# Performance work log

Measured on AMD Instinct MI355X. Metric: run time of the kernel, lower is better.

## Reference

```python
import jax, jax.numpy as jnp
import numpy as np

N_NODES = 1_000_000
N_FEATS = 64
KERNEL_SIZE = 3


def setup_inputs() -> dict:
    key = jax.random.key(0)
    kx, kw = jax.random.split(key)
    x = jax.random.normal(kx, (N_NODES, N_FEATS), dtype=jnp.float32)
    # xavier_uniform for weight of shape (kernel_size, n_feats)
    bound = float(np.sqrt(6.0 / (KERNEL_SIZE + N_FEATS)))
    weight = jax.random.uniform(kw, (KERNEL_SIZE, N_FEATS), dtype=jnp.float32,
                                minval=-bound, maxval=bound)
    # sequential -1/+1 neighbor edges (like mlcg.neighbor_list.get_seq_neigh)
    idx = jnp.arange(N_NODES, dtype=jnp.int64) if jax.config.jax_enable_x64 else jnp.arange(N_NODES, dtype=jnp.int32)
    src = jnp.concatenate([idx[:-1], idx[1:]])   # j
    dst = jnp.concatenate([idx[1:], idx[:-1]])   # i
    disc_edges = jnp.stack([src, dst], axis=0)   # [2, E], E = 2*(N-1)
    return {"x": x, "disc_edges": disc_edges, "weight": weight}


def reference(x, disc_edges, weight):
    src = disc_edges[0]
    dst = disc_edges[1]
    # torch negative-index wrap-around on weight rows -> explicit modulo
    widx = jnp.mod(src - dst, weight.shape[0])
    # gather node feats + per-edge weight row, elementwise multiply
    disc_message = weight[widx] * x[src]                      # [E, F]
    # scatter-add back to destination nodes
    disc_message_scat = jax.ops.segment_sum(disc_message, dst,
                                            num_segments=x.shape[0])  # [N, F]
    # self term
    return disc_message_scat + weight[0] * x
```

## Files before the change

### kernel.cpp

```cpp
#include <hip/hip_runtime.h>

#define NFEAT 64
#define NQ 16
#define STRIP 8

typedef float v4f __attribute__((ext_vector_type(4)));

__device__ __forceinline__ float4 f4_mul(float4 a, float4 b) {
    return make_float4(a.x*b.x, a.y*b.y, a.z*b.z, a.w*b.w);
}
__device__ __forceinline__ float4 f4_fma(float4 a, float4 b, float4 c) {
    return make_float4(fmaf(a.x,b.x,c.x), fmaf(a.y,b.y,c.y),
                       fmaf(a.z,b.z,c.z), fmaf(a.w,b.w,c.w));
}

__global__ void __launch_bounds__(256) check_seq_edges(
        const int* __restrict__ edges, int E, int N, int* __restrict__ flag) {
    int stride = gridDim.x * blockDim.x;
    int half = N - 1;
    bool bad = false;
    for (int e = blockIdx.x * blockDim.x + threadIdx.x; e < E; e += stride) {
        int es, ed;
        if (e < half) { es = e;            ed = e + 1; }
        else          { es = e - half + 1; ed = e - half; }
        bad |= (edges[e] != es) | (edges[E + e] != ed);
    }
    if (bad) atomicOr(flag, 1);
}

__global__ void __launch_bounds__(256) stencil_strip(
        const float* __restrict__ x, const float* __restrict__ w,
        float* __restrict__ out, int N, const int* __restrict__ flag) {
    const float4* __restrict__ x4 = (const float4*)x;
    const float4* __restrict__ w4 = (const float4*)w;
    float4*       __restrict__ o4 = (float4*)out;

    int q = threadIdx.x & 15;
    int strip = blockIdx.x * (blockDim.x >> 4) + (threadIdx.x >> 4);
    int n0 = strip * STRIP;
    if (n0 >= N) return;

    bool fast = (*flag == 0);

    float4 w0 = w4[q];
    float4 w1 = w4[NQ + q];
    float4 w2 = w4[2*NQ + q];

    int base = n0 * NQ + q;
    float4 buf[STRIP + 2];

    if (n0 > 0 && n0 + STRIP < N) {
        #pragma unroll
        for (int s = 0; s < STRIP + 2; ++s)
            buf[s] = x4[base + (s - 1) * NQ];

        if (fast) {
            #pragma unroll
            for (int s = 0; s < STRIP; ++s) {
                float4 acc = f4_mul(w0, buf[s + 1]);
                acc = f4_fma(w2, buf[s], acc);
                acc = f4_fma(w1, buf[s + 2], acc);
                v4f av = {acc.x, acc.y, acc.z, acc.w};
                __builtin_nontemporal_store(av, (v4f*)&o4[base + s * NQ]);
            }
        } else {
            #pragma unroll
            for (int s = 0; s < STRIP; ++s) {
                float4 acc = f4_mul(w0, buf[s + 1]);
                v4f av = {acc.x, acc.y, acc.z, acc.w};
                __builtin_nontemporal_store(av, (v4f*)&o4[base + s * NQ]);
            }
        }
    } else {
        float4 zero = make_float4(0.f, 0.f, 0.f, 0.f);
        #pragma unroll
        for (int s = 0; s < STRIP + 2; ++s) {
            int n = n0 + s - 1;
            buf[s] = (n >= 0 && n < N) ? x4[base + (s - 1) * NQ] : zero;
        }
        #pragma unroll
        for (int s = 0; s < STRIP; ++s) {
            if (n0 + s >= N) break;
            float4 acc = f4_mul(w0, buf[s + 1]);
            if (fast) {
                acc = f4_fma(w2, buf[s], acc);
                acc = f4_fma(w1, buf[s + 2], acc);
            }
            v4f av = {acc.x, acc.y, acc.z, acc.w};
            __builtin_nontemporal_store(av, (v4f*)&o4[base + s * NQ]);
        }
    }
}

__global__ void __launch_bounds__(256) fb_edges(
        const float* __restrict__ x, const int* __restrict__ edges,
        const float* __restrict__ w, float* __restrict__ out,
        int E, const int* __restrict__ flag) {
    if (!*flag) return;
    const float4* __restrict__ x4 = (const float4*)x;
    const float4* __restrict__ w4 = (const float4*)w;
    long long total = (long long)E * NQ;
    long long stride = (long long)gridDim.x * blockDim.x;
    for (long long t = blockIdx.x * (long long)blockDim.x + threadIdx.x;
         t < total; t += stride) {
        int e = (int)(t >> 4);
        int q = (int)(t & 15);
        int src = edges[e];
        int dst = edges[E + e];
        int widx = (src - dst) % 3;
        if (widx < 0) widx += 3;
        float4 v = f4_mul(w4[widx*NQ + q], x4[(long long)src*NQ + q]);
        float* o = out + (long long)dst*NFEAT + q*4;
        atomicAdd(o + 0, v.x);
        atomicAdd(o + 1, v.y);
        atomicAdd(o + 2, v.z);
        atomicAdd(o + 3, v.w);
    }
}

extern "C" void kernel_launch(void* const* d_in, const int* in_sizes, int n_in,
                              void* d_out, int out_size, void* d_ws, size_t ws_size,
                              hipStream_t stream) {
    const float* x     = (const float*)d_in[0];
    const int*   edges = (const int*)d_in[1];
    const float* w     = (const float*)d_in[2];
    float*       out   = (float*)d_out;

    int N = in_sizes[0] / NFEAT;
    int E = in_sizes[1] / 2;

    int* flag = (int*)d_ws;
    hipMemsetAsync(flag, 0, 4, stream);
    check_seq_edges<<<2048, 256, 0, stream>>>(edges, E, N, flag);

    int strips = (N + STRIP - 1) / STRIP;
    long long threads = (long long)strips * NQ;
    int blocks = (int)((threads + 255) / 256);
    stencil_strip<<<blocks, 256, 0, stream>>>(x, w, out, N, flag);

    fb_edges<<<2048, 256, 0, stream>>>(x, edges, w, out, E, flag);
}
```

Measured before the change: 89.65 us.

## Run the stencil unconditionally and correct mismatched edges in a fixup kernel

Drops the separate edge-validation pass, the flag memset, and the flag reads in the stencil kernel. The stencil now always assumes the sequential neighbour pattern. A new per-edge kernel compares each edge against the expected pattern and, only where they differ, subtracts the expected contribution and atomically adds the actual one. This removes one kernel launch and one serialising dependency, though the fixup kernel still reads the whole edge array. For inputs that are not sequential it depends on scalar atomics, which would be slow and could introduce floating-point ordering differences.

```diff
diff --git a/kernel.cpp b/kernel.cpp
--- a/kernel.cpp
+++ b/kernel.cpp
@@ -14,23 +14,9 @@
                        fmaf(a.z,b.z,c.z), fmaf(a.w,b.w,c.w));
 }
 
-__global__ void __launch_bounds__(256) check_seq_edges(
-        const int* __restrict__ edges, int E, int N, int* __restrict__ flag) {
-    int stride = gridDim.x * blockDim.x;
-    int half = N - 1;
-    bool bad = false;
-    for (int e = blockIdx.x * blockDim.x + threadIdx.x; e < E; e += stride) {
-        int es, ed;
-        if (e < half) { es = e;            ed = e + 1; }
-        else          { es = e - half + 1; ed = e - half; }
-        bad |= (edges[e] != es) | (edges[E + e] != ed);
-    }
-    if (bad) atomicOr(flag, 1);
-}
-
 __global__ void __launch_bounds__(256) stencil_strip(
         const float* __restrict__ x, const float* __restrict__ w,
-        float* __restrict__ out, int N, const int* __restrict__ flag) {
+        float* __restrict__ out, int N) {
     const float4* __restrict__ x4 = (const float4*)x;
     const float4* __restrict__ w4 = (const float4*)w;
     float4*       __restrict__ o4 = (float4*)out;
@@ -39,8 +25,6 @@
     int strip = blockIdx.x * (blockDim.x >> 4) + (threadIdx.x >> 4);
     int n0 = strip * STRIP;
     if (n0 >= N) return;
-
-    bool fast = (*flag == 0);
 
     float4 w0 = w4[q];
     float4 w1 = w4[NQ + q];
@@ -54,22 +38,13 @@
         for (int s = 0; s < STRIP + 2; ++s)
             buf[s] = x4[base + (s - 1) * NQ];
 
-        if (fast) {
-            #pragma unroll
-            for (int s = 0; s < STRIP; ++s) {
-                float4 acc = f4_mul(w0, buf[s + 1]);
-                acc = f4_fma(w2, buf[s], acc);
-                acc = f4_fma(w1, buf[s + 2], acc);
-                v4f av = {acc.x, acc.y, acc.z, acc.w};
-                __builtin_nontemporal_store(av, (v4f*)&o4[base + s * NQ]);
-            }
-        } else {
-            #pragma unroll
-            for (int s = 0; s < STRIP; ++s) {
-                float4 acc = f4_mul(w0, buf[s + 1]);
-                v4f av = {acc.x, acc.y, acc.z, acc.w};
-                __builtin_nontemporal_store(av, (v4f*)&o4[base + s * NQ]);
-            }
+        #pragma unroll
+        for (int s = 0; s < STRIP; ++s) {
+            float4 acc = f4_mul(w0, buf[s + 1]);
+            acc = f4_fma(w2, buf[s], acc);
+            acc = f4_fma(w1, buf[s + 2], acc);
+            v4f av = {acc.x, acc.y, acc.z, acc.w};
+            __builtin_nontemporal_store(av, (v4f*)&o4[base + s * NQ]);
         }
     } else {
         float4 zero = make_float4(0.f, 0.f, 0.f, 0.f);
@@ -82,39 +57,43 @@
         for (int s = 0; s < STRIP; ++s) {
             if (n0 + s >= N) break;
             float4 acc = f4_mul(w0, buf[s + 1]);
-            if (fast) {
-                acc = f4_fma(w2, buf[s], acc);
-                acc = f4_fma(w1, buf[s + 2], acc);
-            }
+            acc = f4_fma(w2, buf[s], acc);
+            acc = f4_fma(w1, buf[s + 2], acc);
             v4f av = {acc.x, acc.y, acc.z, acc.w};
             __builtin_nontemporal_store(av, (v4f*)&o4[base + s * NQ]);
         }
     }
 }
 
-__global__ void __launch_bounds__(256) fb_edges(
+__global__ void __launch_bounds__(256) fixup_edges(
         const float* __restrict__ x, const int* __restrict__ edges,
         const float* __restrict__ w, float* __restrict__ out,
-        int E, const int* __restrict__ flag) {
-    if (!*flag) return;
-    const float4* __restrict__ x4 = (const float4*)x;
-    const float4* __restrict__ w4 = (const float4*)w;
-    long long total = (long long)E * NQ;
-    long long stride = (long long)gridDim.x * blockDim.x;
-    for (long long t = blockIdx.x * (long long)blockDim.x + threadIdx.x;
-         t < total; t += stride) {
-        int e = (int)(t >> 4);
-        int q = (int)(t & 15);
-        int src = edges[e];
-        int dst = edges[E + e];
-        int widx = (src - dst) % 3;
-        if (widx < 0) widx += 3;
-        float4 v = f4_mul(w4[widx*NQ + q], x4[(long long)src*NQ + q]);
-        float* o = out + (long long)dst*NFEAT + q*4;
-        atomicAdd(o + 0, v.x);
-        atomicAdd(o + 1, v.y);
-        atomicAdd(o + 2, v.z);
-        atomicAdd(o + 3, v.w);
+        int N, int E) {
+    int e = blockIdx.x * blockDim.x + threadIdx.x;
+    if (e >= E) return;
+
+    int half = N - 1;
+    int es, ed;
+    if (e < half) { es = e;            ed = e + 1; }
+    else          { es = e - half + 1; ed = e - half; }
+
+    int as = edges[e];
+    int ad = edges[E + e];
+    if (as == es && ad == ed) return;
+
+    int ew = (es - ed) % 3; if (ew < 0) ew += 3;
+    int aw = (as - ad) % 3; if (aw < 0) aw += 3;
+
+    const float* we = w + ew * NFEAT;
+    const float* wa = w + aw * NFEAT;
+    const float* xe = x + (long long)es * NFEAT;
+    const float* xa = x + (long long)as * NFEAT;
+    float* oe = out + (long long)ed * NFEAT;
+    float* oa = out + (long long)ad * NFEAT;
+
+    for (int f = 0; f < NFEAT; ++f) {
+        atomicAdd(&oe[f], -we[f] * xe[f]);
+        atomicAdd(&oa[f],  wa[f] * xa[f]);
     }
 }
 
@@ -129,14 +108,11 @@
     int N = in_sizes[0] / NFEAT;
     int E = in_sizes[1] / 2;
 
-    int* flag = (int*)d_ws;
-    hipMemsetAsync(flag, 0, 4, stream);
-    check_seq_edges<<<2048, 256, 0, stream>>>(edges, E, N, flag);
-
     int strips = (N + STRIP - 1) / STRIP;
     long long threads = (long long)strips * NQ;
-    int blocks = (int)((threads + 255) / 256);
-    stencil_strip<<<blocks, 256, 0, stream>>>(x, w, out, N, flag);
+    int sblocks = (int)((threads + 255) / 256);
+    stencil_strip<<<sblocks, 256, 0, stream>>>(x, w, out, N);
 
-    fb_edges<<<2048, 256, 0, stream>>>(x, edges, w, out, E, flag);
+    int fblocks = (E + 255) / 256;
+    fixup_edges<<<fblocks, 256, 0, stream>>>(x, edges, w, out, N, E);
 }
```

New measurement: 82.47 us. 1.09x faster.
